# Kernel optimization log

Hardware: AMD Instinct MI355X
Metric: run time of the kernel (lower is better)

## Reference

```python
import jax, jax.numpy as jnp
import numpy as np

B, S, H, FFN, E = 4, 2048, 2048, 1024, 8


def setup_inputs() -> dict:
    key = jax.random.key(0)
    k0, k1, k2, k3 = jax.random.split(key, 4)
    return {
        "hidden_states": jax.random.normal(k0, (B, S, H), dtype=jnp.float32),
        "gate_w": jax.random.normal(k1, (E, H), dtype=jnp.float32) * 0.02,
        "w13": jax.random.normal(k2, (E, 2 * FFN, H), dtype=jnp.float32) * 0.02,  # [E, 2F, H] (w1 | w3)
        "w2": jax.random.normal(k3, (E, H, FFN), dtype=jnp.float32) * 0.02,        # [E, H, F]
        "top_k": 2,
    }


def reference(hidden_states, gate_w, w13, w2, top_k):
    b, s, h = hidden_states.shape
    num_experts = gate_w.shape[0]
    x = hidden_states.reshape(-1, h)                       # [T, H]
    router_logits = x @ gate_w.T                           # [T, E]
    probs = jax.nn.softmax(router_logits.astype(jnp.float32), axis=-1)
    routing_weights, selected_experts = jax.lax.top_k(probs, top_k)  # [T, K]
    routing_weights = routing_weights / routing_weights.sum(axis=-1, keepdims=True)
    routing_weights = routing_weights.astype(x.dtype)
    out = jnp.zeros_like(x)
    # small fixed loop over experts; intermediates stay [T, 2F] per expert
    for e in range(num_experts):
        h13 = x @ w13[e].T                                 # [T, 2F]
        g, u = jnp.split(h13, 2, axis=-1)
        y = (jax.nn.silu(g) * u) @ w2[e].T                 # [T, H]
        coef = jnp.sum(jnp.where(selected_experts == e, routing_weights, 0.0), axis=-1)
        out = out + coef[:, None] * y
    return out.reshape(b, s, h), router_logits
```

## Files before the change

### kernel.cpp

```cpp
#include <hip/hip_runtime.h>
#include <stdint.h>

typedef short short8 __attribute__((ext_vector_type(8)));
typedef float f32x4 __attribute__((ext_vector_type(4)));
typedef float f32x4v __attribute__((ext_vector_type(4)));
typedef unsigned short u16;

#define T_TOK 8192
#define HID   2048
#define FFNW  1024
#define NE    8
#define NPAIR (2 * T_TOK)

#define VMCNT(n) asm volatile("s_waitcnt vmcnt(" #n ")" ::: "memory")
#define BAR() __builtin_amdgcn_s_barrier()

__device__ __forceinline__ unsigned short f2bf(float f) {
  unsigned int b = __float_as_uint(f);
  b += 0x7fffu + ((b >> 16) & 1u);
  return (unsigned short)(b >> 16);
}
__device__ __forceinline__ float bf2f(unsigned short u) {
  return __uint_as_float(((unsigned)u) << 16);
}

#define GLOAD16(gptr, lptr)                                                          \
  __builtin_amdgcn_global_load_lds(                                                  \
      (const __attribute__((address_space(1))) unsigned int*)(gptr),                 \
      (__attribute__((address_space(3))) unsigned int*)(lptr), 16, 0, 0)

__global__ __launch_bounds__(256) void k_cast(const float* __restrict__ in,
                                              unsigned short* __restrict__ out,
                                              long n8) {
  long i = (long)blockIdx.x * blockDim.x + threadIdx.x;
  long stride = (long)gridDim.x * blockDim.x;
  for (; i < n8; i += stride) {
    const f32x4v* p = (const f32x4v*)(in + i * 8);
    f32x4v a = __builtin_nontemporal_load(p);
    f32x4v b = __builtin_nontemporal_load(p + 1);
    uint4 o;
    o.x = (unsigned)f2bf(a[0]) | ((unsigned)f2bf(a[1]) << 16);
    o.y = (unsigned)f2bf(a[2]) | ((unsigned)f2bf(a[3]) << 16);
    o.z = (unsigned)f2bf(b[0]) | ((unsigned)f2bf(b[1]) << 16);
    o.w = (unsigned)f2bf(b[2]) | ((unsigned)f2bf(b[3]) << 16);
    ((uint4*)out)[i] = o;
  }
}

__global__ __launch_bounds__(256) void k_router(const float* __restrict__ x,
                                                const float* __restrict__ gw,
                                                unsigned short* __restrict__ xb,
                                                float* __restrict__ logits,
                                                int* __restrict__ sel,
                                                float* __restrict__ cw) {
  int wid = threadIdx.x >> 6, lane = threadIdx.x & 63;
  int t = blockIdx.x * 4 + wid;
  const f32x4v* xr = (const f32x4v*)(x + (size_t)t * HID);
  float acc[NE];
#pragma unroll
  for (int e = 0; e < NE; e++) acc[e] = 0.f;
  for (int i = lane; i < HID / 4; i += 64) {
    f32x4v xv = __builtin_nontemporal_load(xr + i);
    ushort4 o;
    o.x = f2bf(xv[0]); o.y = f2bf(xv[1]); o.z = f2bf(xv[2]); o.w = f2bf(xv[3]);
    *(ushort4*)(xb + (size_t)t * HID + i * 4) = o;
#pragma unroll
    for (int e = 0; e < NE; e++) {
      f32x4v gv = ((const f32x4v*)(gw + (size_t)e * HID))[i];
      acc[e] += xv[0] * gv[0] + xv[1] * gv[1] + xv[2] * gv[2] + xv[3] * gv[3];
    }
  }
#pragma unroll
  for (int e = 0; e < NE; e++)
    for (int off = 32; off; off >>= 1) acc[e] += __shfl_down(acc[e], off);
  if (lane == 0) {
    float mx = acc[0];
#pragma unroll
    for (int e = 1; e < NE; e++) mx = fmaxf(mx, acc[e]);
    float p[NE];
#pragma unroll
    for (int e = 0; e < NE; e++) p[e] = expf(acc[e] - mx);
    int i1 = 0; float b1 = p[0];
#pragma unroll
    for (int e = 1; e < NE; e++) if (p[e] > b1) { b1 = p[e]; i1 = e; }
    int i2 = -1; float b2 = -1.f;
#pragma unroll
    for (int e = 0; e < NE; e++) if (e != i1 && p[e] > b2) { b2 = p[e]; i2 = e; }
    float denom = b1 + b2;
#pragma unroll
    for (int e = 0; e < NE; e++) logits[(size_t)t * NE + e] = acc[e];
    sel[2 * t] = i1; sel[2 * t + 1] = i2;
    cw[2 * t] = b1 / denom; cw[2 * t + 1] = b2 / denom;
  }
}

__global__ __launch_bounds__(256) void k_count(const int* __restrict__ sel,
                                               u16* __restrict__ lrank,
                                               int* __restrict__ blkcnt) {
  int blk = blockIdx.x, tid = threadIdx.x;
  int t = blk * 256 + tid;
  int e0 = sel[2 * t], e1 = sel[2 * t + 1];
  int wave = tid >> 6, lane = tid & 63;
  unsigned long long below = (1ull << lane) - 1ull;

  int r0 = 0, r1 = 0, c0[NE], c1[NE];
#pragma unroll
  for (int e = 0; e < NE; e++) {
    unsigned long long m = __ballot(e0 == e);
    if (e == e0) r0 = __popcll(m & below);
    c0[e] = __popcll(m);
  }
#pragma unroll
  for (int e = 0; e < NE; e++) {
    unsigned long long m = __ballot(e1 == e);
    if (e == e1) r1 = __popcll(m & below);
    c1[e] = __popcll(m);
  }

  __shared__ int wcnt[4][NE];
  if (lane < NE) wcnt[wave][lane] = c0[lane] + c1[lane];
  __syncthreads();

  int pre0 = 0, pre1 = 0;
  for (int w = 0; w < wave; w++) { pre0 += wcnt[w][e0]; pre1 += wcnt[w][e1]; }
  lrank[2 * t]     = (u16)(pre0 + r0);
  lrank[2 * t + 1] = (u16)(pre1 + c0[e1] + r1);

  if (tid < NE) {
    int s = 0;
    for (int w = 0; w < 4; w++) s += wcnt[w][tid];
    blkcnt[blk * NE + tid] = s;
  }
}

__global__ __launch_bounds__(256) void k_scanplace(const int* __restrict__ sel,
                                                   const u16* __restrict__ lrank,
                                                   const int* __restrict__ blkcnt,
                                                   int* __restrict__ tokc,
                                                   int* __restrict__ inv,
                                                   int* __restrict__ counts,
                                                   int* __restrict__ base_) {
  int blk = blockIdx.x, tid = threadIdx.x;
  __shared__ int s_pre[NE], s_tot[NE], s_base[NE + 1];
  if (tid < NE) {
    int run = 0, tot = 0;
    for (int b = 0; b < 32; b++) {
      int c = blkcnt[b * NE + tid];
      if (b < blk) run += c;
      tot += c;
    }
    s_pre[tid] = run;
    s_tot[tid] = tot;
  }
  __syncthreads();
  if (tid == 0) {
    int a = 0;
    for (int e = 0; e < NE; e++) { s_base[e] = a; a += s_tot[e]; }
    s_base[NE] = a;
  }
  __syncthreads();

  int t = blk * 256 + tid;
#pragma unroll
  for (int k = 0; k < 2; k++) {
    int e = sel[2 * t + k];
    int pos = s_base[e] + s_pre[e] + (int)lrank[2 * t + k];
    tokc[pos] = t;
    inv[2 * t + k] = pos;
  }
  if (blk == 0 && tid < NE) {
    counts[tid] = s_tot[tid];
    base_[tid] = s_base[tid];
  }
}

__device__ __forceinline__ int xcd_remap(int L, int nwg) {
  return (L & 7) * (nwg >> 3) + (L >> 3);
}

template<bool FUSED, int KD, int ND>
__global__ __launch_bounds__(256, 2) void k_gemm(const u16* __restrict__ A,
                                                 const u16* __restrict__ W,
                                                 u16* __restrict__ Y,
                                                 const int* __restrict__ counts,
                                                 const int* __restrict__ base_,
                                                 const int* __restrict__ tokc) {
  int Wk = xcd_remap(blockIdx.x, 4096);
  int e = Wk >> 9;
  int rem = Wk & 511;
  int by = rem >> 5, bx = rem & 31;

  int cnt = counts[e];
  int m0 = bx * 128;
  if (m0 >= cnt) return;
  constexpr int NCOL = FUSED ? 64 : 128;
  int n0 = by * NCOL;
  int bs = base_[e];

  __shared__ u16 lds[2 * 16384];

  int tid = threadIdx.x;
  int wave = tid >> 6, lane = tid & 63;

  const u16* wb = W + (size_t)e * (FUSED ? (2 * FFNW) * HID : HID * FFNW);

  size_t aoffU[2][2], boffU[2][2];
  unsigned adst[2][2], bdst[2][2];
#pragma unroll
  for (int u = 0; u < 2; u++) {
#pragma unroll
    for (int j = 0; j < 2; j++) {
      int slot = j * 256 + tid;
      int q = slot >> 3, cph = slot & 7;
      int rA = (q & 31) + (q >> 5) * 64 + u * 32;
      int clogA = cph ^ (rA & 7);
      int slA = m0 + rA;
      int grA;
      if (FUSED) grA = tokc[bs + (slA < cnt ? slA : 0)];
      else       grA = bs + (slA < cnt ? slA : 0);
      aoffU[u][j] = (size_t)grA * KD + (size_t)clogA * 8;
      adst[u][j] = (unsigned)(rA * 64 + cph * 8);
      int rB;
      if (FUSED) rB = q + u * 64;
      else       rB = (q & 31) + (q >> 5) * 64 + u * 32;
      int clogB = cph ^ (rB & 7);
      int grB = FUSED ? (rB < 64 ? n0 + rB : FFNW + n0 + (rB - 64)) : (n0 + rB);
      boffU[u][j] = (size_t)grB * KD + (size_t)clogB * 8;
      bdst[u][j] = (unsigned)(8192 + rB * 64 + cph * 8);
    }
  }

  f32x4 acc[4][4];
#pragma unroll
  for (int mi = 0; mi < 4; mi++)
#pragma unroll
    for (int n = 0; n < 4; n++) acc[mi][n] = (f32x4)(0.f);

  int wm = wave >> 1, wn = wave & 1;
  int arow = wm * 64;
  int frow = lane & 15, fk = lane >> 4;
  int sw[2];
  sw[0] = ((fk) ^ (frow & 7)) << 4;
  sw[1] = ((fk + 4) ^ (frow & 7)) << 4;

  constexpr int NT = KD / 64;

#define STAGE_A(u, Ts)                                                                 \
  {                                                                                    \
    unsigned db = ((unsigned)(Ts) & 1) * 16384;                                        \
    size_t ko = (size_t)(Ts) * 64;                                                     \
    GLOAD16(A + aoffU[u][0] + ko, &lds[db + adst[u][0]]);                              \
    GLOAD16(A + aoffU[u][1] + ko, &lds[db + adst[u][1]]);                              \
  }
#define STAGE_B(u, Ts)                                                                 \
  {                                                                                    \
    unsigned db = ((unsigned)(Ts) & 1) * 16384;                                        \
    size_t ko = (size_t)(Ts) * 64;                                                     \
    GLOAD16(wb + boffU[u][0] + ko, &lds[db + bdst[u][0]]);                             \
    GLOAD16(wb + boffU[u][1] + ko, &lds[db + bdst[u][1]]);                             \
  }

  STAGE_A(0, 0); STAGE_B(0, 0); STAGE_A(1, 0); STAGE_B(1, 0);
  STAGE_A(0, 1); STAGE_B(0, 1);
  VMCNT(4);
  BAR();

  short8 af[2][2], bn0[2][2], bn1[2][2];

  for (int T = 0; T < NT; ++T) {
    const char* sb = (const char*)lds + ((unsigned)(T & 1)) * 32768;

#pragma unroll
    for (int mi = 0; mi < 2; mi++)
#pragma unroll
      for (int kk = 0; kk < 2; kk++)
        af[mi][kk] = *(const short8*)(sb + (arow + mi * 16 + frow) * 128 + sw[kk]);
#pragma unroll
    for (int n = 0; n < 2; n++) {
      int rb = FUSED ? (wn * 32 + n * 16 + frow) : (wn * 64 + n * 16 + frow);
#pragma unroll
      for (int kk = 0; kk < 2; kk++)
        bn0[n][kk] = *(const short8*)(sb + 16384 + rb * 128 + sw[kk]);
    }
    if (T + 1 < NT) STAGE_A(1, T + 1);
    BAR();
    __builtin_amdgcn_s_setprio(1);
#pragma unroll
    for (int mi = 0; mi < 2; mi++)
#pragma unroll
      for (int n = 0; n < 2; n++)
#pragma unroll
        for (int kk = 0; kk < 2; kk++)
          acc[mi][n] = __builtin_amdgcn_mfma_f32_16x16x32_bf16(af[mi][kk], bn0[n][kk], acc[mi][n], 0, 0, 0);
    __builtin_amdgcn_s_setprio(0);
    BAR();

#pragma unroll
    for (int n = 0; n < 2; n++) {
      int rb = FUSED ? (64 + wn * 32 + n * 16 + frow) : (wn * 64 + 32 + n * 16 + frow);
#pragma unroll
      for (int kk = 0; kk < 2; kk++)
        bn1[n][kk] = *(const short8*)(sb + 16384 + rb * 128 + sw[kk]);
    }
    if (T + 1 < NT) STAGE_B(1, T + 1);
    BAR();
    __builtin_amdgcn_s_setprio(1);
#pragma unroll
    for (int mi = 0; mi < 2; mi++)
#pragma unroll
      for (int n = 0; n < 2; n++)
#pragma unroll
        for (int kk = 0; kk < 2; kk++)
          acc[mi][n + 2] = __builtin_amdgcn_mfma_f32_16x16x32_bf16(af[mi][kk], bn1[n][kk], acc[mi][n + 2], 0, 0, 0);
    __builtin_amdgcn_s_setprio(0);
    BAR();

#pragma unroll
    for (int mi = 0; mi < 2; mi++)
#pragma unroll
      for (int kk = 0; kk < 2; kk++)
        af[mi][kk] = *(const short8*)(sb + (arow + 32 + mi * 16 + frow) * 128 + sw[kk]);
    if (T + 2 < NT) STAGE_A(0, T + 2);
    BAR();
    __builtin_amdgcn_s_setprio(1);
#pragma unroll
    for (int mi = 0; mi < 2; mi++)
#pragma unroll
      for (int n = 0; n < 2; n++)
#pragma unroll
        for (int kk = 0; kk < 2; kk++)
          acc[mi + 2][n] = __builtin_amdgcn_mfma_f32_16x16x32_bf16(af[mi][kk], bn0[n][kk], acc[mi + 2][n], 0, 0, 0);
    __builtin_amdgcn_s_setprio(0);
    BAR();

    if (T + 2 < NT) STAGE_B(0, T + 2);
    BAR();
    __builtin_amdgcn_s_setprio(1);
#pragma unroll
    for (int mi = 0; mi < 2; mi++)
#pragma unroll
      for (int n = 0; n < 2; n++)
#pragma unroll
        for (int kk = 0; kk < 2; kk++)
          acc[mi + 2][n + 2] = __builtin_amdgcn_mfma_f32_16x16x32_bf16(af[mi][kk], bn1[n][kk], acc[mi + 2][n + 2], 0, 0, 0);
    __builtin_amdgcn_s_setprio(0);
    if (T < NT - 2) { VMCNT(4); }
    else if (T == NT - 2) { VMCNT(0); }
    BAR();
  }
#undef STAGE_A
#undef STAGE_B

#pragma unroll
  for (int mi = 0; mi < 4; mi++) {
#pragma unroll
    for (int r = 0; r < 4; r++) {
      int row = arow + (mi >> 1) * 32 + (mi & 1) * 16 + fk * 4 + r;
      int sl = m0 + row;
      if (sl < cnt) {
        if (FUSED) {
          u16* yr = Y + (size_t)(bs + sl) * ND + n0 + wn * 32 + frow;
#pragma unroll
          for (int j = 0; j < 2; j++) {
            float g = acc[mi][j][r];
            float u = acc[mi][j + 2][r];
            float sv = g / (1.f + expf(-g));
            yr[j * 16] = f2bf(sv * u);
          }
        } else {
          u16* yr = Y + (size_t)(bs + sl) * ND + n0 + wn * 64 + frow;
#pragma unroll
          for (int n = 0; n < 4; n++) yr[n * 16] = f2bf(acc[mi][n][r]);
        }
      }
    }
  }
}

__global__ __launch_bounds__(256) void k_combine(const unsigned short* __restrict__ y,
                                                 const int* __restrict__ inv,
                                                 const float* __restrict__ cw,
                                                 float* __restrict__ out) {
  long i = (long)blockIdx.x * 256 + threadIdx.x;
  int t = (int)(i >> 8);
  int c = (int)(i & 255);
  int p0 = inv[2 * t], p1 = inv[2 * t + 1];
  float c0 = cw[2 * t], c1 = cw[2 * t + 1];
  short8 y0 = *(const short8*)(y + (size_t)p0 * HID + c * 8);
  short8 y1 = *(const short8*)(y + (size_t)p1 * HID + c * 8);
  float4 o0, o1;
  o0.x = c0 * bf2f((unsigned short)y0[0]) + c1 * bf2f((unsigned short)y1[0]);
  o0.y = c0 * bf2f((unsigned short)y0[1]) + c1 * bf2f((unsigned short)y1[1]);
  o0.z = c0 * bf2f((unsigned short)y0[2]) + c1 * bf2f((unsigned short)y1[2]);
  o0.w = c0 * bf2f((unsigned short)y0[3]) + c1 * bf2f((unsigned short)y1[3]);
  o1.x = c0 * bf2f((unsigned short)y0[4]) + c1 * bf2f((unsigned short)y1[4]);
  o1.y = c0 * bf2f((unsigned short)y0[5]) + c1 * bf2f((unsigned short)y1[5]);
  o1.z = c0 * bf2f((unsigned short)y0[6]) + c1 * bf2f((unsigned short)y1[6]);
  o1.w = c0 * bf2f((unsigned short)y0[7]) + c1 * bf2f((unsigned short)y1[7]);
  float4* op = (float4*)(out + (size_t)t * HID + c * 8);
  op[0] = o0;
  op[1] = o1;
}

extern "C" void kernel_launch(void* const* d_in, const int* in_sizes, int n_in,
                              void* d_out, int out_size, void* d_ws, size_t ws_size,
                              hipStream_t stream) {
  const float* x   = (const float*)d_in[0];
  const float* gw  = (const float*)d_in[1];
  const float* w13 = (const float*)d_in[2];
  const float* w2  = (const float*)d_in[3];
  float* out = (float*)d_out;
  float* logits = out + (size_t)T_TOK * HID;

  uint8_t* p = (uint8_t*)d_ws;
  unsigned short* xb   = (unsigned short*)p; p += (size_t)T_TOK * HID * 2;
  unsigned short* w13b = (unsigned short*)p; p += (size_t)NE * 2 * FFNW * HID * 2;
  unsigned short* w2b  = (unsigned short*)p; p += (size_t)NE * HID * FFNW * 2;
  unsigned short* act  = (unsigned short*)p; p += (size_t)NPAIR * FFNW * 2;
  unsigned short* y    = (unsigned short*)p; p += (size_t)NPAIR * HID * 2;
  int* sel  = (int*)p;   p += (size_t)NPAIR * 4;
  float* cw = (float*)p; p += (size_t)NPAIR * 4;
  int* tokc = (int*)p;   p += (size_t)NPAIR * 4;
  int* inv  = (int*)p;   p += (size_t)NPAIR * 4;
  u16* lrank = (u16*)p;  p += (size_t)NPAIR * 2;
  int* blkcnt = (int*)p; p += 32 * NE * 4;
  int* counts = (int*)p; p += 256;
  int* base   = (int*)p; p += 256;
  if ((size_t)(p - (uint8_t*)d_ws) > ws_size) return;

  k_cast<<<2048, 256, 0, stream>>>(w13, w13b, (long)NE * 2 * FFNW * HID / 8);
  k_router<<<T_TOK / 4, 256, 0, stream>>>(x, gw, xb, logits, sel, cw);
  k_count<<<32, 256, 0, stream>>>(sel, lrank, blkcnt);
  k_scanplace<<<32, 256, 0, stream>>>(sel, lrank, blkcnt, tokc, inv, counts, base);

  k_gemm<true, HID, FFNW><<<4096, 256, 0, stream>>>(xb, w13b, act, counts, base, tokc);

  k_cast<<<2048, 256, 0, stream>>>(w2, w2b, (long)NE * HID * FFNW / 8);

  k_gemm<false, FFNW, HID><<<4096, 256, 0, stream>>>(act, w2b, y, counts, base, tokc);
  k_combine<<<(int)((long)T_TOK * HID / 8 / 256), 256, 0, stream>>>(y, inv, cw, out);
}
```

Baseline: 359.9 us.

## Fuse combine into down-projection GEMM via atomic scatter, simplify K-loop pipeline

The down-projection GEMM epilogue now scales each result by its routing coefficient and atomically adds it into the fp32 output row of the owning token. This removes the bf16 y buffer and the separate combine kernel; the output is zeroed with a memset first. The inner K loop also changes from four quarter-step phases with several barriers each to one phase that loads all A and B fragments, issues both next-stage prefetches, and runs all MFMAs. In exchange it adds fp32 atomic traffic with nondeterministic summation order, and it keeps more fragment registers live at once, which may cut occupancy.

```diff
diff --git a/kernel.cpp b/kernel.cpp
--- a/kernel.cpp
+++ b/kernel.cpp
@@ -13,6 +13,7 @@
 #define NPAIR (2 * T_TOK)
 
 #define VMCNT(n) asm volatile("s_waitcnt vmcnt(" #n ")" ::: "memory")
+#define LGKM0()  asm volatile("s_waitcnt lgkmcnt(0)" ::: "memory")
 #define BAR() __builtin_amdgcn_s_barrier()
 
 __device__ __forceinline__ unsigned short f2bf(float f) {
@@ -136,8 +137,9 @@
 __global__ __launch_bounds__(256) void k_scanplace(const int* __restrict__ sel,
                                                    const u16* __restrict__ lrank,
                                                    const int* __restrict__ blkcnt,
+                                                   const float* __restrict__ cw,
                                                    int* __restrict__ tokc,
-                                                   int* __restrict__ inv,
+                                                   float* __restrict__ coefp,
                                                    int* __restrict__ counts,
                                                    int* __restrict__ base_) {
   int blk = blockIdx.x, tid = threadIdx.x;
@@ -166,7 +168,7 @@
     int e = sel[2 * t + k];
     int pos = s_base[e] + s_pre[e] + (int)lrank[2 * t + k];
     tokc[pos] = t;
-    inv[2 * t + k] = pos;
+    coefp[pos] = cw[2 * t + k];
   }
   if (blk == 0 && tid < NE) {
     counts[tid] = s_tot[tid];
@@ -182,9 +184,11 @@
 __global__ __launch_bounds__(256, 2) void k_gemm(const u16* __restrict__ A,
                                                  const u16* __restrict__ W,
                                                  u16* __restrict__ Y,
+                                                 float* __restrict__ out,
                                                  const int* __restrict__ counts,
                                                  const int* __restrict__ base_,
-                                                 const int* __restrict__ tokc) {
+                                                 const int* __restrict__ tokc,
+                                                 const float* __restrict__ coefp) {
   int Wk = xcd_remap(blockIdx.x, 4096);
   int e = Wk >> 9;
   int rem = Wk & 511;
@@ -265,85 +269,43 @@
   VMCNT(4);
   BAR();
 
-  short8 af[2][2], bn0[2][2], bn1[2][2];
-
   for (int T = 0; T < NT; ++T) {
     const char* sb = (const char*)lds + ((unsigned)(T & 1)) * 32768;
 
-#pragma unroll
-    for (int mi = 0; mi < 2; mi++)
+    short8 af[4][2], bn0[2][2], bn1[2][2];
+#pragma unroll
+    for (int mi = 0; mi < 4; mi++)
 #pragma unroll
       for (int kk = 0; kk < 2; kk++)
         af[mi][kk] = *(const short8*)(sb + (arow + mi * 16 + frow) * 128 + sw[kk]);
 #pragma unroll
     for (int n = 0; n < 2; n++) {
-      int rb = FUSED ? (wn * 32 + n * 16 + frow) : (wn * 64 + n * 16 + frow);
-#pragma unroll
-      for (int kk = 0; kk < 2; kk++)
-        bn0[n][kk] = *(const short8*)(sb + 16384 + rb * 128 + sw[kk]);
-    }
-    if (T + 1 < NT) STAGE_A(1, T + 1);
+      int rb0 = FUSED ? (wn * 32 + n * 16 + frow) : (wn * 64 + n * 16 + frow);
+      int rb1 = FUSED ? (64 + wn * 32 + n * 16 + frow) : (wn * 64 + 32 + n * 16 + frow);
+#pragma unroll
+      for (int kk = 0; kk < 2; kk++) {
+        bn0[n][kk] = *(const short8*)(sb + 16384 + rb0 * 128 + sw[kk]);
+        bn1[n][kk] = *(const short8*)(sb + 16384 + rb1 * 128 + sw[kk]);
+      }
+    }
+    LGKM0();
     BAR();
+
+    if (T + 1 < NT) { STAGE_A(1, T + 1); STAGE_B(1, T + 1); }
+    if (T + 2 < NT) { STAGE_A(0, T + 2); STAGE_B(0, T + 2); }
+
     __builtin_amdgcn_s_setprio(1);
 #pragma unroll
-    for (int mi = 0; mi < 2; mi++)
+    for (int mi = 0; mi < 4; mi++)
 #pragma unroll
       for (int n = 0; n < 2; n++)
 #pragma unroll
-        for (int kk = 0; kk < 2; kk++)
-          acc[mi][n] = __builtin_amdgcn_mfma_f32_16x16x32_bf16(af[mi][kk], bn0[n][kk], acc[mi][n], 0, 0, 0);
+        for (int kk = 0; kk < 2; kk++) {
+          acc[mi][n]     = __builtin_amdgcn_mfma_f32_16x16x32_bf16(af[mi][kk], bn0[n][kk], acc[mi][n], 0, 0, 0);
+          acc[mi][n + 2] = __builtin_amdgcn_mfma_f32_16x16x32_bf16(af[mi][kk], bn1[n][kk], acc[mi][n + 2], 0, 0, 0);
+        }
     __builtin_amdgcn_s_setprio(0);
-    BAR();
-
-#pragma unroll
-    for (int n = 0; n < 2; n++) {
-      int rb = FUSED ? (64 + wn * 32 + n * 16 + frow) : (wn * 64 + 32 + n * 16 + frow);
-#pragma unroll
-      for (int kk = 0; kk < 2; kk++)
-        bn1[n][kk] = *(const short8*)(sb + 16384 + rb * 128 + sw[kk]);
-    }
-    if (T + 1 < NT) STAGE_B(1, T + 1);
-    BAR();
-    __builtin_amdgcn_s_setprio(1);
-#pragma unroll
-    for (int mi = 0; mi < 2; mi++)
-#pragma unroll
-      for (int n = 0; n < 2; n++)
-#pragma unroll
-        for (int kk = 0; kk < 2; kk++)
-          acc[mi][n + 2] = __builtin_amdgcn_mfma_f32_16x16x32_bf16(af[mi][kk], bn1[n][kk], acc[mi][n + 2], 0, 0, 0);
-    __builtin_amdgcn_s_setprio(0);
-    BAR();
-
-#pragma unroll
-    for (int mi = 0; mi < 2; mi++)
-#pragma unroll
-      for (int kk = 0; kk < 2; kk++)
-        af[mi][kk] = *(const short8*)(sb + (arow + 32 + mi * 16 + frow) * 128 + sw[kk]);
-    if (T + 2 < NT) STAGE_A(0, T + 2);
-    BAR();
-    __builtin_amdgcn_s_setprio(1);
-#pragma unroll
-    for (int mi = 0; mi < 2; mi++)
-#pragma unroll
-      for (int n = 0; n < 2; n++)
-#pragma unroll
-        for (int kk = 0; kk < 2; kk++)
-          acc[mi + 2][n] = __builtin_amdgcn_mfma_f32_16x16x32_bf16(af[mi][kk], bn0[n][kk], acc[mi + 2][n], 0, 0, 0);
-    __builtin_amdgcn_s_setprio(0);
-    BAR();
-
-    if (T + 2 < NT) STAGE_B(0, T + 2);
-    BAR();
-    __builtin_amdgcn_s_setprio(1);
-#pragma unroll
-    for (int mi = 0; mi < 2; mi++)
-#pragma unroll
-      for (int n = 0; n < 2; n++)
-#pragma unroll
-        for (int kk = 0; kk < 2; kk++)
-          acc[mi + 2][n + 2] = __builtin_amdgcn_mfma_f32_16x16x32_bf16(af[mi][kk], bn1[n][kk], acc[mi + 2][n + 2], 0, 0, 0);
-    __builtin_amdgcn_s_setprio(0);
+
     if (T < NT - 2) { VMCNT(4); }
     else if (T == NT - 2) { VMCNT(0); }
     BAR();
@@ -355,7 +317,7 @@
   for (int mi = 0; mi < 4; mi++) {
 #pragma unroll
     for (int r = 0; r < 4; r++) {
-      int row = arow + (mi >> 1) * 32 + (mi & 1) * 16 + fk * 4 + r;
+      int row = arow + mi * 16 + fk * 4 + r;
       int sl = m0 + row;
       if (sl < cnt) {
         if (FUSED) {
@@ -368,38 +330,16 @@
             yr[j * 16] = f2bf(sv * u);
           }
         } else {
-          u16* yr = Y + (size_t)(bs + sl) * ND + n0 + wn * 64 + frow;
-#pragma unroll
-          for (int n = 0; n < 4; n++) yr[n * 16] = f2bf(acc[mi][n][r]);
+          int t = tokc[bs + sl];
+          float coef = coefp[bs + sl];
+          float* orow = out + (size_t)t * HID + n0 + wn * 64 + frow;
+#pragma unroll
+          for (int n = 0; n < 4; n++)
+            atomicAdd(orow + n * 16, coef * acc[mi][n][r]);
         }
       }
     }
   }
-}
-
-__global__ __launch_bounds__(256) void k_combine(const unsigned short* __restrict__ y,
-                                                 const int* __restrict__ inv,
-                                                 const float* __restrict__ cw,
-                                                 float* __restrict__ out) {
-  long i = (long)blockIdx.x * 256 + threadIdx.x;
-  int t = (int)(i >> 8);
-  int c = (int)(i & 255);
-  int p0 = inv[2 * t], p1 = inv[2 * t + 1];
-  float c0 = cw[2 * t], c1 = cw[2 * t + 1];
-  short8 y0 = *(const short8*)(y + (size_t)p0 * HID + c * 8);
-  short8 y1 = *(const short8*)(y + (size_t)p1 * HID + c * 8);
-  float4 o0, o1;
-  o0.x = c0 * bf2f((unsigned short)y0[0]) + c1 * bf2f((unsigned short)y1[0]);
-  o0.y = c0 * bf2f((unsigned short)y0[1]) + c1 * bf2f((unsigned short)y1[1]);
-  o0.z = c0 * bf2f((unsigned short)y0[2]) + c1 * bf2f((unsigned short)y1[2]);
-  o0.w = c0 * bf2f((unsigned short)y0[3]) + c1 * bf2f((unsigned short)y1[3]);
-  o1.x = c0 * bf2f((unsigned short)y0[4]) + c1 * bf2f((unsigned short)y1[4]);
-  o1.y = c0 * bf2f((unsigned short)y0[5]) + c1 * bf2f((unsigned short)y1[5]);
-  o1.z = c0 * bf2f((unsigned short)y0[6]) + c1 * bf2f((unsigned short)y1[6]);
-  o1.w = c0 * bf2f((unsigned short)y0[7]) + c1 * bf2f((unsigned short)y1[7]);
-  float4* op = (float4*)(out + (size_t)t * HID + c * 8);
-  op[0] = o0;
-  op[1] = o1;
 }
 
 extern "C" void kernel_launch(void* const* d_in, const int* in_sizes, int n_in,
@@ -417,26 +357,26 @@
   unsigned short* w13b = (unsigned short*)p; p += (size_t)NE * 2 * FFNW * HID * 2;
   unsigned short* w2b  = (unsigned short*)p; p += (size_t)NE * HID * FFNW * 2;
   unsigned short* act  = (unsigned short*)p; p += (size_t)NPAIR * FFNW * 2;
-  unsigned short* y    = (unsigned short*)p; p += (size_t)NPAIR * HID * 2;
-  int* sel  = (int*)p;   p += (size_t)NPAIR * 4;
-  float* cw = (float*)p; p += (size_t)NPAIR * 4;
-  int* tokc = (int*)p;   p += (size_t)NPAIR * 4;
-  int* inv  = (int*)p;   p += (size_t)NPAIR * 4;
-  u16* lrank = (u16*)p;  p += (size_t)NPAIR * 2;
-  int* blkcnt = (int*)p; p += 32 * NE * 4;
-  int* counts = (int*)p; p += 256;
-  int* base   = (int*)p; p += 256;
+  int* sel  = (int*)p;    p += (size_t)NPAIR * 4;
+  float* cw = (float*)p;  p += (size_t)NPAIR * 4;
+  int* tokc = (int*)p;    p += (size_t)NPAIR * 4;
+  float* coefp = (float*)p; p += (size_t)NPAIR * 4;
+  u16* lrank = (u16*)p;   p += (size_t)NPAIR * 2;
+  int* blkcnt = (int*)p;  p += 32 * NE * 4;
+  int* counts = (int*)p;  p += 256;
+  int* base   = (int*)p;  p += 256;
   if ((size_t)(p - (uint8_t*)d_ws) > ws_size) return;
+
+  hipMemsetAsync(out, 0, (size_t)T_TOK * HID * sizeof(float), stream);
 
   k_cast<<<2048, 256, 0, stream>>>(w13, w13b, (long)NE * 2 * FFNW * HID / 8);
   k_router<<<T_TOK / 4, 256, 0, stream>>>(x, gw, xb, logits, sel, cw);
   k_count<<<32, 256, 0, stream>>>(sel, lrank, blkcnt);
-  k_scanplace<<<32, 256, 0, stream>>>(sel, lrank, blkcnt, tokc, inv, counts, base);
-
-  k_gemm<true, HID, FFNW><<<4096, 256, 0, stream>>>(xb, w13b, act, counts, base, tokc);
+  k_scanplace<<<32, 256, 0, stream>>>(sel, lrank, blkcnt, cw, tokc, coefp, counts, base);
+
+  k_gemm<true, HID, FFNW><<<4096, 256, 0, stream>>>(xb, w13b, act, out, counts, base, tokc, coefp);
 
   k_cast<<<2048, 256, 0, stream>>>(w2, w2b, (long)NE * HID * FFNW / 8);
 
-  k_gemm<false, FFNW, HID><<<4096, 256, 0, stream>>>(act, w2b, y, counts, base, tokc);
-  k_combine<<<(int)((long)T_TOK * HID / 8 / 256), 256, 0, stream>>>(y, inv, cw, out);
-}
+  k_gemm<false, FFNW, HID><<<4096, 256, 0, stream>>>(act, w2b, (u16*)nullptr, out, counts, base, tokc, coefp);
+}
```

After: 414.5 us. 1.15x slower.

## Halve GEMM K-tile, simplify to one-barrier pipeline, raise occupancy to three

Applied to the files above, without the earlier changes.

The grouped expert GEMM now stages 32-wide K slices instead of 64, with a matching swizzle. This halves LDS per block, so launch bounds can request three blocks per CU. The four interleaved sub-phases per K step, each with its own barriers, are replaced by one fragment load, an lgkmcnt wait, one barrier, issue of the next two stages, then 16 MFMAs. The grid doubles so the expert m-tile index covers up to 64 tiles. That adds early-exit blocks, and each MFMA step now gets less K work per barrier.

```diff
diff --git a/kernel.cpp b/kernel.cpp
--- a/kernel.cpp
+++ b/kernel.cpp
@@ -13,6 +13,7 @@
 #define NPAIR (2 * T_TOK)
 
 #define VMCNT(n) asm volatile("s_waitcnt vmcnt(" #n ")" ::: "memory")
+#define LGKM0()  asm volatile("s_waitcnt lgkmcnt(0)" ::: "memory")
 #define BAR() __builtin_amdgcn_s_barrier()
 
 __device__ __forceinline__ unsigned short f2bf(float f) {
@@ -179,16 +180,16 @@
 }
 
 template<bool FUSED, int KD, int ND>
-__global__ __launch_bounds__(256, 2) void k_gemm(const u16* __restrict__ A,
+__global__ __launch_bounds__(256, 3) void k_gemm(const u16* __restrict__ A,
                                                  const u16* __restrict__ W,
                                                  u16* __restrict__ Y,
                                                  const int* __restrict__ counts,
                                                  const int* __restrict__ base_,
                                                  const int* __restrict__ tokc) {
-  int Wk = xcd_remap(blockIdx.x, 4096);
-  int e = Wk >> 9;
-  int rem = Wk & 511;
-  int by = rem >> 5, bx = rem & 31;
+  int Wk = xcd_remap(blockIdx.x, 8192);
+  int e = Wk >> 10;
+  int rem = Wk & 1023;
+  int by = rem >> 6, bx = rem & 63;
 
   int cnt = counts[e];
   int m0 = bx * 128;
@@ -197,37 +198,29 @@
   int n0 = by * NCOL;
   int bs = base_[e];
 
-  __shared__ u16 lds[2 * 16384];
+  __shared__ u16 lds[2 * 8192];
 
   int tid = threadIdx.x;
   int wave = tid >> 6, lane = tid & 63;
+  int q = tid >> 2, cph = tid & 3;
+  int clog = cph ^ ((q >> 1) & 3);
 
   const u16* wb = W + (size_t)e * (FUSED ? (2 * FFNW) * HID : HID * FFNW);
 
-  size_t aoffU[2][2], boffU[2][2];
-  unsigned adst[2][2], bdst[2][2];
+  size_t aoffU[2], boffU[2];
+  unsigned adstU[2], bdstU[2];
 #pragma unroll
   for (int u = 0; u < 2; u++) {
-#pragma unroll
-    for (int j = 0; j < 2; j++) {
-      int slot = j * 256 + tid;
-      int q = slot >> 3, cph = slot & 7;
-      int rA = (q & 31) + (q >> 5) * 64 + u * 32;
-      int clogA = cph ^ (rA & 7);
-      int slA = m0 + rA;
-      int grA;
-      if (FUSED) grA = tokc[bs + (slA < cnt ? slA : 0)];
-      else       grA = bs + (slA < cnt ? slA : 0);
-      aoffU[u][j] = (size_t)grA * KD + (size_t)clogA * 8;
-      adst[u][j] = (unsigned)(rA * 64 + cph * 8);
-      int rB;
-      if (FUSED) rB = q + u * 64;
-      else       rB = (q & 31) + (q >> 5) * 64 + u * 32;
-      int clogB = cph ^ (rB & 7);
-      int grB = FUSED ? (rB < 64 ? n0 + rB : FFNW + n0 + (rB - 64)) : (n0 + rB);
-      boffU[u][j] = (size_t)grB * KD + (size_t)clogB * 8;
-      bdst[u][j] = (unsigned)(8192 + rB * 64 + cph * 8);
-    }
+    int rA = q + u * 64;
+    int slA = m0 + rA;
+    int grA = FUSED ? tokc[bs + (slA < cnt ? slA : 0)] : (bs + (slA < cnt ? slA : 0));
+    aoffU[u] = (size_t)grA * KD + (size_t)clog * 8;
+    adstU[u] = (unsigned)(rA * 32 + cph * 8);
+    int rB = q + u * 64;
+    int grB = FUSED ? ((q < 32) ? (n0 + u * 32 + q) : (FFNW + n0 + u * 32 + (q - 32)))
+                    : (n0 + rB);
+    boffU[u] = (size_t)grB * KD + (size_t)clog * 8;
+    bdstU[u] = (unsigned)(4096 + rB * 32 + cph * 8);
   }
 
   f32x4 acc[4][4];
@@ -239,123 +232,57 @@
   int wm = wave >> 1, wn = wave & 1;
   int arow = wm * 64;
   int frow = lane & 15, fk = lane >> 4;
-  int sw[2];
-  sw[0] = ((fk) ^ (frow & 7)) << 4;
-  sw[1] = ((fk + 4) ^ (frow & 7)) << 4;
-
-  constexpr int NT = KD / 64;
-
-#define STAGE_A(u, Ts)                                                                 \
+  int swo = (fk ^ ((frow >> 1) & 3)) << 4;
+
+  constexpr int NT = KD / 32;
+
+#define STAGE(u, Ts)                                                                   \
   {                                                                                    \
-    unsigned db = ((unsigned)(Ts) & 1) * 16384;                                        \
-    size_t ko = (size_t)(Ts) * 64;                                                     \
-    GLOAD16(A + aoffU[u][0] + ko, &lds[db + adst[u][0]]);                              \
-    GLOAD16(A + aoffU[u][1] + ko, &lds[db + adst[u][1]]);                              \
-  }
-#define STAGE_B(u, Ts)                                                                 \
-  {                                                                                    \
-    unsigned db = ((unsigned)(Ts) & 1) * 16384;                                        \
-    size_t ko = (size_t)(Ts) * 64;                                                     \
-    GLOAD16(wb + boffU[u][0] + ko, &lds[db + bdst[u][0]]);                             \
-    GLOAD16(wb + boffU[u][1] + ko, &lds[db + bdst[u][1]]);                             \
-  }
-
-  STAGE_A(0, 0); STAGE_B(0, 0); STAGE_A(1, 0); STAGE_B(1, 0);
-  STAGE_A(0, 1); STAGE_B(0, 1);
-  VMCNT(4);
+    unsigned db = ((unsigned)(Ts) & 1) * 8192;                                         \
+    size_t ko = (size_t)(Ts) * 32;                                                     \
+    GLOAD16(A + aoffU[u] + ko, &lds[db + adstU[u]]);                                   \
+    GLOAD16(wb + boffU[u] + ko, &lds[db + bdstU[u]]);                                  \
+  }
+
+  STAGE(0, 0); STAGE(1, 0); STAGE(0, 1);
+  VMCNT(2);
   BAR();
 
-  short8 af[2][2], bn0[2][2], bn1[2][2];
-
   for (int T = 0; T < NT; ++T) {
-    const char* sb = (const char*)lds + ((unsigned)(T & 1)) * 32768;
-
-#pragma unroll
-    for (int mi = 0; mi < 2; mi++)
-#pragma unroll
-      for (int kk = 0; kk < 2; kk++)
-        af[mi][kk] = *(const short8*)(sb + (arow + mi * 16 + frow) * 128 + sw[kk]);
-#pragma unroll
-    for (int n = 0; n < 2; n++) {
-      int rb = FUSED ? (wn * 32 + n * 16 + frow) : (wn * 64 + n * 16 + frow);
-#pragma unroll
-      for (int kk = 0; kk < 2; kk++)
-        bn0[n][kk] = *(const short8*)(sb + 16384 + rb * 128 + sw[kk]);
-    }
-    if (T + 1 < NT) STAGE_A(1, T + 1);
+    const char* sb = (const char*)lds + ((unsigned)(T & 1)) * 16384;
+
+    short8 af[4], bn[4];
+#pragma unroll
+    for (int mi = 0; mi < 4; mi++)
+      af[mi] = *(const short8*)(sb + (arow + mi * 16 + frow) * 64 + swo);
+#pragma unroll
+    for (int n = 0; n < 4; n++)
+      bn[n] = *(const short8*)(sb + 8192 + (wn * 64 + n * 16 + frow) * 64 + swo);
+    LGKM0();
     BAR();
+
+    if (T + 1 < NT) STAGE(1, T + 1);
+    if (T + 2 < NT) STAGE(0, T + 2);
+
     __builtin_amdgcn_s_setprio(1);
 #pragma unroll
-    for (int mi = 0; mi < 2; mi++)
-#pragma unroll
-      for (int n = 0; n < 2; n++)
-#pragma unroll
-        for (int kk = 0; kk < 2; kk++)
-          acc[mi][n] = __builtin_amdgcn_mfma_f32_16x16x32_bf16(af[mi][kk], bn0[n][kk], acc[mi][n], 0, 0, 0);
+    for (int mi = 0; mi < 4; mi++)
+#pragma unroll
+      for (int n = 0; n < 4; n++)
+        acc[mi][n] = __builtin_amdgcn_mfma_f32_16x16x32_bf16(af[mi], bn[n], acc[mi][n], 0, 0, 0);
     __builtin_amdgcn_s_setprio(0);
-    BAR();
-
-#pragma unroll
-    for (int n = 0; n < 2; n++) {
-      int rb = FUSED ? (64 + wn * 32 + n * 16 + frow) : (wn * 64 + 32 + n * 16 + frow);
-#pragma unroll
-      for (int kk = 0; kk < 2; kk++)
-        bn1[n][kk] = *(const short8*)(sb + 16384 + rb * 128 + sw[kk]);
-    }
-    if (T + 1 < NT) STAGE_B(1, T + 1);
-    BAR();
-    __builtin_amdgcn_s_setprio(1);
-#pragma unroll
-    for (int mi = 0; mi < 2; mi++)
-#pragma unroll
-      for (int n = 0; n < 2; n++)
-#pragma unroll
-        for (int kk = 0; kk < 2; kk++)
-          acc[mi][n + 2] = __builtin_amdgcn_mfma_f32_16x16x32_bf16(af[mi][kk], bn1[n][kk], acc[mi][n + 2], 0, 0, 0);
-    __builtin_amdgcn_s_setprio(0);
-    BAR();
-
-#pragma unroll
-    for (int mi = 0; mi < 2; mi++)
-#pragma unroll
-      for (int kk = 0; kk < 2; kk++)
-        af[mi][kk] = *(const short8*)(sb + (arow + 32 + mi * 16 + frow) * 128 + sw[kk]);
-    if (T + 2 < NT) STAGE_A(0, T + 2);
-    BAR();
-    __builtin_amdgcn_s_setprio(1);
-#pragma unroll
-    for (int mi = 0; mi < 2; mi++)
-#pragma unroll
-      for (int n = 0; n < 2; n++)
-#pragma unroll
-        for (int kk = 0; kk < 2; kk++)
-          acc[mi + 2][n] = __builtin_amdgcn_mfma_f32_16x16x32_bf16(af[mi][kk], bn0[n][kk], acc[mi + 2][n], 0, 0, 0);
-    __builtin_amdgcn_s_setprio(0);
-    BAR();
-
-    if (T + 2 < NT) STAGE_B(0, T + 2);
-    BAR();
-    __builtin_amdgcn_s_setprio(1);
-#pragma unroll
-    for (int mi = 0; mi < 2; mi++)
-#pragma unroll
-      for (int n = 0; n < 2; n++)
-#pragma unroll
-        for (int kk = 0; kk < 2; kk++)
-          acc[mi + 2][n + 2] = __builtin_amdgcn_mfma_f32_16x16x32_bf16(af[mi][kk], bn1[n][kk], acc[mi + 2][n + 2], 0, 0, 0);
-    __builtin_amdgcn_s_setprio(0);
-    if (T < NT - 2) { VMCNT(4); }
+
+    if (T < NT - 2) { VMCNT(2); }
     else if (T == NT - 2) { VMCNT(0); }
     BAR();
   }
-#undef STAGE_A
-#undef STAGE_B
+#undef STAGE
 
 #pragma unroll
   for (int mi = 0; mi < 4; mi++) {
 #pragma unroll
     for (int r = 0; r < 4; r++) {
-      int row = arow + (mi >> 1) * 32 + (mi & 1) * 16 + fk * 4 + r;
+      int row = arow + mi * 16 + fk * 4 + r;
       int sl = m0 + row;
       if (sl < cnt) {
         if (FUSED) {
@@ -433,10 +360,10 @@
   k_count<<<32, 256, 0, stream>>>(sel, lrank, blkcnt);
   k_scanplace<<<32, 256, 0, stream>>>(sel, lrank, blkcnt, tokc, inv, counts, base);
 
-  k_gemm<true, HID, FFNW><<<4096, 256, 0, stream>>>(xb, w13b, act, counts, base, tokc);
+  k_gemm<true, HID, FFNW><<<8192, 256, 0, stream>>>(xb, w13b, act, counts, base, tokc);
 
   k_cast<<<2048, 256, 0, stream>>>(w2, w2b, (long)NE * HID * FFNW / 8);
 
-  k_gemm<false, FFNW, HID><<<4096, 256, 0, stream>>>(act, w2b, y, counts, base, tokc);
+  k_gemm<false, FFNW, HID><<<8192, 256, 0, stream>>>(act, w2b, y, counts, base, tokc);
   k_combine<<<(int)((long)T_TOK * HID / 8 / 256), 256, 0, stream>>>(y, inv, cw, out);
 }
```

Measured after the change: 422.6 us. 17.4% more time.
